# Performance work log

Hardware: AMD Instinct MI355X
Metric: run time of the kernel (lower is better)

Reference implementation:

```python
import jax, jax.numpy as jnp
import numpy as np

NUM_CONTROL_POINTS = 4
# Standard Catmull-Rom spline basis (rows map [1, t, t^2, t^3] monomials to control points)
CATMULL_ROM_BASIS = 0.5 * np.array(
    [[0.0, 2.0, 0.0, 0.0],
     [-1.0, 0.0, 1.0, 0.0],
     [2.0, -5.0, 4.0, -1.0],
     [-1.0, 3.0, -3.0, 1.0]], dtype=np.float32)

BATCH, IN_F, OUT_F = 1024, 512, 512


def setup_inputs() -> dict:
    key = jax.random.key(0)
    k1, k2, k3, k4 = jax.random.split(key, 4)
    inp = jax.random.normal(k1, (BATCH, IN_F), dtype=jnp.float32)
    # phase spans [0, 2*pi) so both spline segments (mask = phase < 1.5*pi) are exercised
    phase = jax.random.uniform(k2, (BATCH,), dtype=jnp.float32) * (2.0 * jnp.pi)
    bound = 1.0 / np.sqrt(IN_F)
    weights = jax.random.uniform(k3, (NUM_CONTROL_POINTS, OUT_F, IN_F), dtype=jnp.float32,
                                 minval=-bound, maxval=bound)
    biases = jax.random.uniform(k4, (NUM_CONTROL_POINTS, OUT_F), dtype=jnp.float32,
                                minval=-bound, maxval=bound)
    return {"input": inp, "phase": phase, "weights": weights, "biases": biases}


def _spline_coeffs(phase):
    # Faithful to the original (including its overwrite bug): tt = [1, t^2, t^3, 0]
    basis = jnp.asarray(CATMULL_ROM_BASIS, dtype=phase.dtype)
    t0 = phase / (1.5 * jnp.pi)
    t1 = (phase - 0.5 * jnp.pi) / (1.5 * jnp.pi)
    ones, zeros = jnp.ones_like(phase), jnp.zeros_like(phase)
    tt0 = jnp.stack([ones, t0 * t0, t0 ** 3, zeros], axis=1)  # (B,4)
    tt1 = jnp.stack([ones, t1 * t1, t1 ** 3, zeros], axis=1)  # (B,4)
    mask = (phase < 1.5 * jnp.pi)[:, None]
    # Selecting per-sample coefficients before the weight contraction is exactly
    # equivalent to where(mask, tt0@B@W, tt1@B@W) since the map is linear in tt.
    return jnp.where(mask, tt0 @ basis, tt1 @ basis)  # (B,4) control-point coeffs


def reference(input, phase, weights, biases):
    c = _spline_coeffs(phase)                       # (B,4)
    # Fused form: apply the 4 shared control-point linear layers, then blend,
    # avoiding the (B,out,in) per-sample weight tensor. Same math as
    # (tt@B@W).reshape(B,out,in) @ input[:,:,None] + b.
    y4 = jnp.einsum('bi,coi->bco', input, weights)  # (B,4,out)
    out = jnp.einsum('bc,bco->bo', c, y4) + c @ biases  # (B,out)
    return out
```

## Files before the change

kernel.cpp:

```cpp
#include <hip/hip_runtime.h>


#define BATCH 1024
#define IN_F  512
#define OUT_F 512

constexpr int BM = 32;
constexpr int BO = 16;
constexpr int BK = 32;
constexpr int KW = IN_F / 2;
constexpr int KITERS = KW / BK;
constexpr int A_ELEMS = 2 * BM * BK;
constexpr int W_ELEMS = 2 * 4 * BO * BK;
constexpr int TILE_ELEMS = A_ELEMS + W_ELEMS;
constexpr int NVEC = TILE_ELEMS / 8;

typedef unsigned short u16;
typedef u16    u16x8  __attribute__((ext_vector_type(8)));
typedef __bf16 bf16x8 __attribute__((ext_vector_type(8)));
typedef float  f32x4  __attribute__((ext_vector_type(4)));

__device__ __forceinline__ u16 f2bits(float f) {
  union { float f; unsigned int u; } v; v.f = f;
  unsigned int u = v.u;
  unsigned int r = u + 0x7fffu + ((u >> 16) & 1u);
  return (u16)(r >> 16);
}

__global__ __launch_bounds__(256)
void PhaseLinear_kernel(const float* __restrict__ inp, const float* __restrict__ ph,
                        const float* __restrict__ wts, const float* __restrict__ bia,
                        float* __restrict__ outp) {
  __shared__ alignas(16) u16 sT[2][TILE_ELEMS];
  __shared__ float sCoef[BM][4];
  __shared__ float sRed[2][64][16];

  const int tid = threadIdx.x;
  const int wv  = tid >> 6;
  const int wm  = wv & 1;
  const int ks  = wv >> 1;
  const int l   = tid & 63;
  const int o0  = blockIdx.x * BO;
  const int b0  = blockIdx.y * BM;

  if (tid < BM) {
    const float PI = 3.14159265358979323846f;
    float p  = ph[b0 + tid];
    float t  = (p < 1.5f * PI) ? (p / (1.5f * PI)) : ((p - 0.5f * PI) / (1.5f * PI));
    float t2 = t * t, t3 = t2 * t;
    sCoef[tid][0] = t3 - 0.5f * t2;
    sCoef[tid][1] = 1.0f - 2.5f * t3;
    sCoef[tid][2] = 0.5f * t2 + 2.0f * t3;
    sCoef[tid][3] = -0.5f * t3;
  }

  const float* src[3];
  int loff[3];
#pragma unroll
  for (int j = 0; j < 3; ++j) {
    int v = tid + j * 256;
    int e = v * 8;
    loff[j] = e;
    if (e < A_ELEMS) {
      int w = e >> 10, rem = e & 1023;
      int row = rem >> 5, k = rem & 31;
      src[j] = inp + (size_t)(b0 + row) * IN_F + w * KW + k;
    } else {
      int e2 = e - A_ELEMS;
      int w = e2 >> 11, rem = e2 & 2047;
      int r = rem >> 5, k = rem & 31;
      int c = r >> 4, oo = r & 15;
      src[j] = wts + ((size_t)c * OUT_F + o0 + oo) * IN_F + w * KW + k;
    }
  }

  f32x4 regs[3][2];
#pragma unroll
  for (int j = 0; j < 3; ++j) {
    regs[j][0] = *(const f32x4*)(src[j]);
    regs[j][1] = *(const f32x4*)(src[j] + 4);
  }

  f32x4 acc[4];
#pragma unroll
  for (int c = 0; c < 4; ++c) acc[c] = (f32x4){0.f, 0.f, 0.f, 0.f};

  const int q = l >> 4;
  const int n = l & 15;

  for (int kk = 0; kk < KITERS; ++kk) {
    const int bsel = kk & 1;
    u16* buf = &sT[bsel][0];
#pragma unroll
    for (int j = 0; j < 3; ++j) {
      u16x8 pk;
#pragma unroll
      for (int x = 0; x < 4; ++x) {
        pk[x]     = f2bits(regs[j][0][x]);
        pk[x + 4] = f2bits(regs[j][1][x]);
      }
      *(u16x8*)(buf + loff[j]) = pk;
    }
    if (kk + 1 < KITERS) {
#pragma unroll
      for (int j = 0; j < 3; ++j) {
        regs[j][0] = *(const f32x4*)(src[j] + (kk + 1) * BK);
        regs[j][1] = *(const f32x4*)(src[j] + (kk + 1) * BK + 4);
      }
    }
    __syncthreads();
    bf16x8 a0 = *(const bf16x8*)(buf + ks * 1024 + (wm * 16 + n) * BK + q * 8);
    const u16* pW = buf + A_ELEMS + ks * 2048;
#pragma unroll
    for (int c = 0; c < 4; ++c) {
      bf16x8 wf = *(const bf16x8*)(pW + c * 512 + n * BK + q * 8);
      acc[c] = __builtin_amdgcn_mfma_f32_16x16x32_bf16(a0, wf, acc[c], 0, 0, 0);
    }
  }

  if (ks == 1) {
#pragma unroll
    for (int c = 0; c < 4; ++c)
#pragma unroll
      for (int r = 0; r < 4; ++r) sRed[wm][l][c * 4 + r] = acc[c][r];
  }
  __syncthreads();
  if (ks == 0) {
    const int o = o0 + n;
    float bs[4];
#pragma unroll
    for (int c = 0; c < 4; ++c) bs[c] = bia[c * OUT_F + o];

#pragma unroll
    for (int r = 0; r < 4; ++r) {
      const int bl = wm * 16 + q * 4 + r;
      float v = 0.f;
#pragma unroll
      for (int c = 0; c < 4; ++c) {
        float s = acc[c][r] + sRed[wm][l][c * 4 + r];
        v += sCoef[bl][c] * (s + bs[c]);
      }
      outp[(size_t)(b0 + bl) * OUT_F + o] = v;
    }
  }
}

extern "C" void kernel_launch(void* const* d_in, const int* in_sizes, int n_in,
                              void* d_out, int out_size, void* d_ws, size_t ws_size,
                              hipStream_t stream) {
  const float* inp = (const float*)d_in[0];
  const float* ph  = (const float*)d_in[1];
  const float* wts = (const float*)d_in[2];
  const float* bia = (const float*)d_in[3];
  float* outp = (float*)d_out;

  dim3 grid(OUT_F / BO, BATCH / BM);
  PhaseLinear_kernel<<<grid, 256, 0, stream>>>(inp, ph, wts, bia, outp);
}
```

Measured before the change: 72.56 us.

## Pre-convert inputs and weights to bf16 MFMA fragment layout in separate kernel

Adds a conversion kernel that turns the fp32 input and weights into bf16, stored in the workspace in MFMA-fragment order. The main GEMM kernel then loads fragments straight from global memory into registers with double buffering, with no shared-memory staging and no per-tile barriers. It uses 128 threads per block with two k-split waves, and each wave now covers two 16-row M tiles. This removes the repeated fp32-to-bf16 conversion across blocks and the LDS round trip, at the cost of a second launch and an extra pass through the workspace.

After: 70.54 us. -2.8%, faster.

```diff
diff --git a/kernel.cpp b/kernel.cpp
--- a/kernel.cpp
+++ b/kernel.cpp
@@ -5,20 +5,13 @@
 #define IN_F  512
 #define OUT_F 512
 
-constexpr int BM = 32;
-constexpr int BO = 16;
-constexpr int BK = 32;
-constexpr int KW = IN_F / 2;
-constexpr int KITERS = KW / BK;
-constexpr int A_ELEMS = 2 * BM * BK;
-constexpr int W_ELEMS = 2 * 4 * BO * BK;
-constexpr int TILE_ELEMS = A_ELEMS + W_ELEMS;
-constexpr int NVEC = TILE_ELEMS / 8;
-
 typedef unsigned short u16;
 typedef u16    u16x8  __attribute__((ext_vector_type(8)));
 typedef __bf16 bf16x8 __attribute__((ext_vector_type(8)));
 typedef float  f32x4  __attribute__((ext_vector_type(4)));
+
+#define A_GRANULES 65536
+#define W_GRANULES 131072
 
 __device__ __forceinline__ u16 f2bits(float f) {
   union { float f; unsigned int u; } v; v.f = f;
@@ -28,119 +21,120 @@
 }
 
 __global__ __launch_bounds__(256)
-void PhaseLinear_kernel(const float* __restrict__ inp, const float* __restrict__ ph,
-                        const float* __restrict__ wts, const float* __restrict__ bia,
-                        float* __restrict__ outp) {
-  __shared__ alignas(16) u16 sT[2][TILE_ELEMS];
-  __shared__ float sCoef[BM][4];
-  __shared__ float sRed[2][64][16];
+void Convert_kernel(const float* __restrict__ inp, const float* __restrict__ wts,
+                    u16x8* __restrict__ ws) {
+  const int s = blockIdx.x * 256 + threadIdx.x;
+  const float* src;
+  if (s < A_GRANULES) {
+    const int frag = s >> 6, l = s & 63;
+    const int btile = frag >> 4, kblk = frag & 15;
+    const int m = l & 15, qq = l >> 4;
+    src = inp + (size_t)(btile * 16 + m) * IN_F + kblk * 32 + qq * 8;
+  } else {
+    const int t = s - A_GRANULES;
+    const int frag = t >> 6, l = t & 63;
+    const int kblk = frag & 15, rest = frag >> 4;
+    const int c = rest & 3, otile = rest >> 2;
+    const int n = l & 15, qq = l >> 4;
+    src = wts + ((size_t)c * OUT_F + otile * 16 + n) * IN_F + kblk * 32 + qq * 8;
+  }
+  const f32x4 v0 = *(const f32x4*)src;
+  const f32x4 v1 = *(const f32x4*)(src + 4);
+  u16x8 pk;
+#pragma unroll
+  for (int x = 0; x < 4; ++x) {
+    pk[x]     = f2bits(v0[x]);
+    pk[x + 4] = f2bits(v1[x]);
+  }
+  ws[s] = pk;
+}
+
+__global__ __launch_bounds__(128)
+void PhaseLinear_kernel(const u16x8* __restrict__ ws, const float* __restrict__ ph,
+                        const float* __restrict__ bia, float* __restrict__ outp) {
+  __shared__ f32x4 sRed[8][64];
 
   const int tid = threadIdx.x;
-  const int wv  = tid >> 6;
-  const int wm  = wv & 1;
-  const int ks  = wv >> 1;
+  const int ks  = tid >> 6;
   const int l   = tid & 63;
-  const int o0  = blockIdx.x * BO;
-  const int b0  = blockIdx.y * BM;
+  const int q   = l >> 4;
+  const int n   = l & 15;
+  const int otile = blockIdx.x;
+  const int bty   = blockIdx.y;
 
-  if (tid < BM) {
-    const float PI = 3.14159265358979323846f;
-    float p  = ph[b0 + tid];
-    float t  = (p < 1.5f * PI) ? (p / (1.5f * PI)) : ((p - 0.5f * PI) / (1.5f * PI));
-    float t2 = t * t, t3 = t2 * t;
-    sCoef[tid][0] = t3 - 0.5f * t2;
-    sCoef[tid][1] = 1.0f - 2.5f * t3;
-    sCoef[tid][2] = 0.5f * t2 + 2.0f * t3;
-    sCoef[tid][3] = -0.5f * t3;
-  }
+  const bf16x8* __restrict__ A  = (const bf16x8*)ws;
+  const bf16x8* __restrict__ Wp = (const bf16x8*)ws + A_GRANULES;
 
-  const float* src[3];
-  int loff[3];
+  const int ai0 = ((bty * 2 + 0) * 16 + ks * 8) * 64 + l;
+  const int ai1 = ((bty * 2 + 1) * 16 + ks * 8) * 64 + l;
+  int wi[4];
 #pragma unroll
-  for (int j = 0; j < 3; ++j) {
-    int v = tid + j * 256;
-    int e = v * 8;
-    loff[j] = e;
-    if (e < A_ELEMS) {
-      int w = e >> 10, rem = e & 1023;
-      int row = rem >> 5, k = rem & 31;
-      src[j] = inp + (size_t)(b0 + row) * IN_F + w * KW + k;
-    } else {
-      int e2 = e - A_ELEMS;
-      int w = e2 >> 11, rem = e2 & 2047;
-      int r = rem >> 5, k = rem & 31;
-      int c = r >> 4, oo = r & 15;
-      src[j] = wts + ((size_t)c * OUT_F + o0 + oo) * IN_F + w * KW + k;
+  for (int c = 0; c < 4; ++c) wi[c] = ((otile * 4 + c) * 16 + ks * 8) * 64 + l;
+
+  bf16x8 a[2][2], w[2][4];
+  a[0][0] = A[ai0];
+  a[0][1] = A[ai1];
+#pragma unroll
+  for (int c = 0; c < 4; ++c) w[0][c] = Wp[wi[c]];
+
+  f32x4 acc[2][4];
+#pragma unroll
+  for (int mi = 0; mi < 2; ++mi)
+#pragma unroll
+    for (int c = 0; c < 4; ++c) acc[mi][c] = (f32x4){0.f, 0.f, 0.f, 0.f};
+
+#pragma unroll
+  for (int kk = 0; kk < 8; ++kk) {
+    const int cb = kk & 1, nb = cb ^ 1;
+    if (kk < 7) {
+      const int off = (kk + 1) * 64;
+      a[nb][0] = A[ai0 + off];
+      a[nb][1] = A[ai1 + off];
+#pragma unroll
+      for (int c = 0; c < 4; ++c) w[nb][c] = Wp[wi[c] + off];
     }
-  }
-
-  f32x4 regs[3][2];
 #pragma unroll
-  for (int j = 0; j < 3; ++j) {
-    regs[j][0] = *(const f32x4*)(src[j]);
-    regs[j][1] = *(const f32x4*)(src[j] + 4);
-  }
-
-  f32x4 acc[4];
+    for (int mi = 0; mi < 2; ++mi)
 #pragma unroll
-  for (int c = 0; c < 4; ++c) acc[c] = (f32x4){0.f, 0.f, 0.f, 0.f};
-
-  const int q = l >> 4;
-  const int n = l & 15;
-
-  for (int kk = 0; kk < KITERS; ++kk) {
-    const int bsel = kk & 1;
-    u16* buf = &sT[bsel][0];
-#pragma unroll
-    for (int j = 0; j < 3; ++j) {
-      u16x8 pk;
-#pragma unroll
-      for (int x = 0; x < 4; ++x) {
-        pk[x]     = f2bits(regs[j][0][x]);
-        pk[x + 4] = f2bits(regs[j][1][x]);
-      }
-      *(u16x8*)(buf + loff[j]) = pk;
-    }
-    if (kk + 1 < KITERS) {
-#pragma unroll
-      for (int j = 0; j < 3; ++j) {
-        regs[j][0] = *(const f32x4*)(src[j] + (kk + 1) * BK);
-        regs[j][1] = *(const f32x4*)(src[j] + (kk + 1) * BK + 4);
-      }
-    }
-    __syncthreads();
-    bf16x8 a0 = *(const bf16x8*)(buf + ks * 1024 + (wm * 16 + n) * BK + q * 8);
-    const u16* pW = buf + A_ELEMS + ks * 2048;
-#pragma unroll
-    for (int c = 0; c < 4; ++c) {
-      bf16x8 wf = *(const bf16x8*)(pW + c * 512 + n * BK + q * 8);
-      acc[c] = __builtin_amdgcn_mfma_f32_16x16x32_bf16(a0, wf, acc[c], 0, 0, 0);
-    }
+      for (int c = 0; c < 4; ++c)
+        acc[mi][c] = __builtin_amdgcn_mfma_f32_16x16x32_bf16(a[cb][mi], w[cb][c],
+                                                             acc[mi][c], 0, 0, 0);
   }
 
   if (ks == 1) {
 #pragma unroll
-    for (int c = 0; c < 4; ++c)
+    for (int mi = 0; mi < 2; ++mi)
 #pragma unroll
-      for (int r = 0; r < 4; ++r) sRed[wm][l][c * 4 + r] = acc[c][r];
+      for (int c = 0; c < 4; ++c) sRed[mi * 4 + c][l] = acc[mi][c];
   }
   __syncthreads();
+
   if (ks == 0) {
-    const int o = o0 + n;
+    const float PI = 3.14159265358979323846f;
+    const int o = otile * 16 + n;
     float bs[4];
 #pragma unroll
     for (int c = 0; c < 4; ++c) bs[c] = bia[c * OUT_F + o];
 
 #pragma unroll
-    for (int r = 0; r < 4; ++r) {
-      const int bl = wm * 16 + q * 4 + r;
-      float v = 0.f;
+    for (int mi = 0; mi < 2; ++mi) {
 #pragma unroll
-      for (int c = 0; c < 4; ++c) {
-        float s = acc[c][r] + sRed[wm][l][c * 4 + r];
-        v += sCoef[bl][c] * (s + bs[c]);
+      for (int r = 0; r < 4; ++r) {
+        const int b = bty * 32 + mi * 16 + q * 4 + r;
+        const float p  = ph[b];
+        const float t  = (p < 1.5f * PI) ? (p / (1.5f * PI)) : ((p - 0.5f * PI) / (1.5f * PI));
+        const float t2 = t * t, t3 = t2 * t;
+        const float c0 = t3 - 0.5f * t2;
+        const float c1 = 1.0f - 2.5f * t3;
+        const float c2 = 0.5f * t2 + 2.0f * t3;
+        const float c3 = -0.5f * t3;
+        const float s0 = acc[mi][0][r] + sRed[mi * 4 + 0][l][r];
+        const float s1 = acc[mi][1][r] + sRed[mi * 4 + 1][l][r];
+        const float s2 = acc[mi][2][r] + sRed[mi * 4 + 2][l][r];
+        const float s3 = acc[mi][3][r] + sRed[mi * 4 + 3][l][r];
+        outp[(size_t)b * OUT_F + o] =
+            c0 * (s0 + bs[0]) + c1 * (s1 + bs[1]) + c2 * (s2 + bs[2]) + c3 * (s3 + bs[3]);
       }
-      outp[(size_t)(b0 + bl) * OUT_F + o] = v;
     }
   }
 }
@@ -154,6 +148,9 @@
   const float* bia = (const float*)d_in[3];
   float* outp = (float*)d_out;
 
-  dim3 grid(OUT_F / BO, BATCH / BM);
-  PhaseLinear_kernel<<<grid, 256, 0, stream>>>(inp, ph, wts, bia, outp);
+  Convert_kernel<<<dim3((A_GRANULES + W_GRANULES) / 256), 256, 0, stream>>>(
+      inp, wts, (u16x8*)d_ws);
+
+  dim3 grid(OUT_F / 16, BATCH / 32);
+  PhaseLinear_kernel<<<grid, 128, 0, stream>>>((const u16x8*)d_ws, ph, bia, outp);
 }
```
